# Optimization experiments

Measured on AMD Instinct MI355X. Metric: run time of the kernel, lower is better.

The kernel has to match this reference:

```python
import jax, jax.numpy as jnp
import numpy as np

N = 8192
D_IN, D_GAT, D_GCN = 128, 64, 64


def setup_inputs() -> dict:
    key = jax.random.key(0)
    ks = jax.random.split(key, 7)
    feat = jax.random.normal(ks[0], (N, D_IN), dtype=jnp.float32)
    r = jax.random.uniform(ks[1], (N, N), dtype=jnp.float32)
    sup = jnp.where(r < 0.01, r * 100.0, 0.0)
    xav = lambda k, shape: jax.random.normal(k, shape, dtype=jnp.float32) * jnp.sqrt(2.0 / (shape[0] + shape[1]))
    W_map = xav(ks[2], (D_IN, D_GAT))
    b_map = jnp.zeros((1,), dtype=jnp.float32)
    U = xav(ks[3], (D_GAT, 1))
    V = xav(ks[4], (D_GAT, 1))
    W_gcn = xav(ks[5], (D_GAT, D_GCN))
    return {"feat": feat, "sup": sup, "W_map": W_map, "b_map": b_map, "U": U, "V": V, "W_gcn": W_gcn}


def reference(feat, sup, W_map, b_map, U, V, W_gcn):
    n = sup.shape[0]
    sup2 = sup + jnp.eye(n, dtype=sup.dtype)  # add self-loops
    # GAT layer
    h = feat @ W_map                            # [N, D_GAT]
    s = h @ U                                   # [N, 1] score from source node i
    t = h @ V                                   # [N, 1] score from target node j
    # torch loop builds att[j, i] = tanh(s_i + t_j + b)
    att = jnp.tanh(s.T + t + b_map)             # [N, N]
    att = jnp.where(sup2 > 0, att, jnp.float32(-100.0))
    att = jax.nn.softmax(att, axis=1)
    gat_feat = jnp.tanh(att @ h)                # [N, D_GAT]
    # GCN layer (dropout is identity at inference)
    agg = sup2 @ gat_feat                       # [N, D_GAT]
    out = jax.nn.relu(agg @ W_gcn)              # [N, D_GCN]
    norm = jnp.linalg.norm(out, axis=1, keepdims=True)
    out = out / jnp.maximum(norm, jnp.float32(1e-12))  # F.normalize(p=2, dim=1)
    return out
```

## Files before the change

### kernel.cpp

```cpp
#include <hip/hip_runtime.h>
#include <hip/hip_bf16.h>


#define N_NODES 8192
#define D_IN    128
#define D_GAT   64
#define SLOTS   256
#define K1_BLOCKS (N_NODES / 4)

__global__ __launch_bounds__(256) void k12_map_compact(
    const float* __restrict__ feat, const float* __restrict__ W_map,
    const float* __restrict__ U, const float* __restrict__ V,
    const float* __restrict__ sup,
    float* __restrict__ h, float* __restrict__ s, float* __restrict__ t,
    int* __restrict__ cnt, int* __restrict__ col, float* __restrict__ val)
{
    if (blockIdx.x < K1_BLOCKS) {
        const int r = threadIdx.x >> 6;
        const int d = threadIdx.x & 63;
        const int row = blockIdx.x * 4 + r;
        __shared__ float f[4 * D_IN];
        if (threadIdx.x < 128)
            ((float4*)f)[threadIdx.x] =
                ((const float4*)(feat + (size_t)blockIdx.x * 4 * D_IN))[threadIdx.x];
        __syncthreads();
        const float* fr = f + r * D_IN;
        float acc = 0.f;
#pragma unroll 8
        for (int k = 0; k < D_IN; ++k)
            acc += fr[k] * W_map[k * D_GAT + d];
        h[row * D_GAT + d] = acc;
        float sv = acc * U[d];
        float tv = acc * V[d];
#pragma unroll
        for (int off = 32; off > 0; off >>= 1) {
            sv += __shfl_xor(sv, off);
            tv += __shfl_xor(tv, off);
        }
        if (d == 0) { s[row] = sv; t[row] = tv; }
    } else {
        const int j = blockIdx.x - K1_BLOCKS;
        const int lane = threadIdx.x & 63;
        __shared__ int c;
        if (threadIdx.x == 0) c = 0;
        __syncthreads();
        const float4* row = (const float4*)(sup + (size_t)j * N_NODES);
        int*   colj = col + j * SLOTS;
        float* valj = val + j * SLOTS;
        for (int q = threadIdx.x; q < N_NODES / 4; q += 256) {
            float4 v = row[q];
            const int i0 = q * 4;
            float vs[4] = {v.x, v.y, v.z, v.w};
#pragma unroll
            for (int u = 0; u < 4; ++u) {
                const int i = i0 + u;
                const float vv = vs[u] + ((i == j) ? 1.0f : 0.0f);
                const bool keep = vv > 0.f;
                const unsigned long long mask = __ballot(keep);
                if (mask) {
                    int base = 0;
                    if (lane == 0) base = atomicAdd(&c, __popcll(mask));
                    base = __shfl(base, 0);
                    if (keep) {
                        const int pos = base +
                            __popcll(mask & ((1ull << lane) - 1ull));
                        if (pos < SLOTS) { colj[pos] = i; valj[pos] = vv; }
                    }
                }
            }
        }
        __syncthreads();
        if (threadIdx.x == 0) cnt[j] = (c < SLOTS) ? c : SLOTS;
    }
}

__global__ __launch_bounds__(256) void k3_gat(
    const float* __restrict__ h, const float* __restrict__ s,
    const float* __restrict__ t, const float* __restrict__ b,
    const int* __restrict__ cnt, const int* __restrict__ col,
    float* __restrict__ gat)
{
    const int wid  = threadIdx.x >> 6;
    const int lane = threadIdx.x & 63;
    const int j = blockIdx.x * 4 + wid;
    const int m = cnt[j];
    const int* colj = col + j * SLOTS;
    __shared__ int   cl_s[4][SLOTS];
    __shared__ float w_s[4][SLOTS];
    int*   cl = cl_s[wid];
    float* w  = w_s[wid];
    const float tj = t[j] + b[0];

    float lmax = -1e30f;
    for (int p = lane; p < m; p += 64) {
        const int ci = colj[p];
        cl[p] = ci;
        const float e = tanhf(s[ci] + tj);
        w[p] = e;
        lmax = fmaxf(lmax, e);
    }
#pragma unroll
    for (int off = 32; off > 0; off >>= 1)
        lmax = fmaxf(lmax, __shfl_xor(lmax, off));

    float lsum = 0.f;
    for (int p = lane; p < m; p += 64) {
        const float e = __expf(w[p] - lmax);
        w[p] = e;
        lsum += e;
    }
#pragma unroll
    for (int off = 32; off > 0; off >>= 1) lsum += __shfl_xor(lsum, off);
    __syncthreads();

    const int c16 = (lane & 15) * 4;
    const int pp  = lane >> 4;
    float4 a0 = make_float4(0,0,0,0), a1 = a0, a2 = a0, a3 = a0;
    for (int base = 0; base < m; base += 16) {
        const int p0 = base + pp, p1 = p0 + 4, p2 = p0 + 8, p3 = p0 + 12;
        if (p0 < m) { const float wp = w[p0];
            const float4 v = *(const float4*)(h + cl[p0] * D_GAT + c16);
            a0.x += wp*v.x; a0.y += wp*v.y; a0.z += wp*v.z; a0.w += wp*v.w; }
        if (p1 < m) { const float wp = w[p1];
            const float4 v = *(const float4*)(h + cl[p1] * D_GAT + c16);
            a1.x += wp*v.x; a1.y += wp*v.y; a1.z += wp*v.z; a1.w += wp*v.w; }
        if (p2 < m) { const float wp = w[p2];
            const float4 v = *(const float4*)(h + cl[p2] * D_GAT + c16);
            a2.x += wp*v.x; a2.y += wp*v.y; a2.z += wp*v.z; a2.w += wp*v.w; }
        if (p3 < m) { const float wp = w[p3];
            const float4 v = *(const float4*)(h + cl[p3] * D_GAT + c16);
            a3.x += wp*v.x; a3.y += wp*v.y; a3.z += wp*v.z; a3.w += wp*v.w; }
    }
    float4 acc;
    acc.x = (a0.x + a1.x) + (a2.x + a3.x);
    acc.y = (a0.y + a1.y) + (a2.y + a3.y);
    acc.z = (a0.z + a1.z) + (a2.z + a3.z);
    acc.w = (a0.w + a1.w) + (a2.w + a3.w);
#pragma unroll
    for (int off = 16; off <= 32; off <<= 1) {
        acc.x += __shfl_xor(acc.x, off); acc.y += __shfl_xor(acc.y, off);
        acc.z += __shfl_xor(acc.z, off); acc.w += __shfl_xor(acc.w, off);
    }
    if (pp == 0) {
        const float inv = 1.0f / lsum;
        float4 o;
        o.x = tanhf(acc.x * inv); o.y = tanhf(acc.y * inv);
        o.z = tanhf(acc.z * inv); o.w = tanhf(acc.w * inv);
        *(float4*)(gat + j * D_GAT + c16) = o;
    }
}

__global__ __launch_bounds__(256) void k4_gcn(
    const float* __restrict__ gat, const float* __restrict__ W_gcn,
    const int* __restrict__ cnt, const int* __restrict__ col,
    const float* __restrict__ val, float* __restrict__ out)
{
    const int wid  = threadIdx.x >> 6;
    const int lane = threadIdx.x & 63;
    const int j = blockIdx.x * 4 + wid;
    const int m = cnt[j];
    const int*   colj = col + j * SLOTS;
    const float* valj = val + j * SLOTS;
    __shared__ int   cl_s[4][SLOTS];
    __shared__ float wv_s[4][SLOTS];
    __shared__ float a_s[4][D_GAT];
    int*   cl = cl_s[wid];
    float* wv = wv_s[wid];
    float* a  = a_s[wid];
    for (int p = lane; p < m; p += 64) { cl[p] = colj[p]; wv[p] = valj[p]; }
    __syncthreads();

    const int c16 = (lane & 15) * 4;
    const int pp  = lane >> 4;
    float4 a0 = make_float4(0,0,0,0), a1 = a0, a2 = a0, a3 = a0;
    for (int base = 0; base < m; base += 16) {
        const int p0 = base + pp, p1 = p0 + 4, p2 = p0 + 8, p3 = p0 + 12;
        if (p0 < m) { const float wp = wv[p0];
            const float4 v = *(const float4*)(gat + cl[p0] * D_GAT + c16);
            a0.x += wp*v.x; a0.y += wp*v.y; a0.z += wp*v.z; a0.w += wp*v.w; }
        if (p1 < m) { const float wp = wv[p1];
            const float4 v = *(const float4*)(gat + cl[p1] * D_GAT + c16);
            a1.x += wp*v.x; a1.y += wp*v.y; a1.z += wp*v.z; a1.w += wp*v.w; }
        if (p2 < m) { const float wp = wv[p2];
            const float4 v = *(const float4*)(gat + cl[p2] * D_GAT + c16);
            a2.x += wp*v.x; a2.y += wp*v.y; a2.z += wp*v.z; a2.w += wp*v.w; }
        if (p3 < m) { const float wp = wv[p3];
            const float4 v = *(const float4*)(gat + cl[p3] * D_GAT + c16);
            a3.x += wp*v.x; a3.y += wp*v.y; a3.z += wp*v.z; a3.w += wp*v.w; }
    }
    float4 acc;
    acc.x = (a0.x + a1.x) + (a2.x + a3.x);
    acc.y = (a0.y + a1.y) + (a2.y + a3.y);
    acc.z = (a0.z + a1.z) + (a2.z + a3.z);
    acc.w = (a0.w + a1.w) + (a2.w + a3.w);
#pragma unroll
    for (int off = 16; off <= 32; off <<= 1) {
        acc.x += __shfl_xor(acc.x, off); acc.y += __shfl_xor(acc.y, off);
        acc.z += __shfl_xor(acc.z, off); acc.w += __shfl_xor(acc.w, off);
    }
    if (pp == 0) *(float4*)(a + c16) = acc;
    __syncthreads();

    float o = 0.f;
#pragma unroll 8
    for (int d = 0; d < D_GAT; ++d)
        o += a[d] * W_gcn[d * D_GAT + lane];
    o = fmaxf(o, 0.f);

    float ss = o * o;
#pragma unroll
    for (int off = 32; off > 0; off >>= 1) ss += __shfl_xor(ss, off);
    const float nrm = sqrtf(ss);
    out[j * D_GAT + lane] = o / fmaxf(nrm, 1e-12f);
}

extern "C" void kernel_launch(void* const* d_in, const int* in_sizes, int n_in,
                              void* d_out, int out_size, void* d_ws, size_t ws_size,
                              hipStream_t stream) {
    const float* feat  = (const float*)d_in[0];
    const float* sup   = (const float*)d_in[1];
    const float* W_map = (const float*)d_in[2];
    const float* b_map = (const float*)d_in[3];
    const float* U     = (const float*)d_in[4];
    const float* V     = (const float*)d_in[5];
    const float* W_gcn = (const float*)d_in[6];
    float* out = (float*)d_out;

    char* ws = (char*)d_ws;
    float* h   = (float*)(ws);
    float* gat = (float*)(ws + (2u << 20));
    float* s   = (float*)(ws + (4u << 20));
    float* t   = (float*)(ws + (4u << 20) + 32768);
    int*   cnt = (int*)  (ws + (4u << 20) + 65536);
    int*   col = (int*)  (ws + (4u << 20) + 98304);
    float* val = (float*)(ws + (12u << 20) + 98304);

    k12_map_compact<<<K1_BLOCKS + N_NODES, 256, 0, stream>>>(
        feat, W_map, U, V, sup, h, s, t, cnt, col, val);
    k3_gat<<<N_NODES / 4, 256, 0, stream>>>(h, s, t, b_map, cnt, col, gat);
    k4_gcn<<<N_NODES / 4, 256, 0, stream>>>(gat, W_gcn, cnt, col, val, out);
}
```

Before: 408.8 us.

## Compact adjacency per-wave segments without shared atomics, issue all row loads upfront

The sparse-compaction stage now gives each of the four waves its own 64-slot segment of a row with a per-wave count, so the shared-memory atomic, the broadcast shuffle and the block barriers go away. Each wave issues its eight float4 loads of the dense row before processing them, which raises memory-level parallelism on the 256 MB adjacency scan. The consumer kernels merge the four segments into shared memory using the per-wave counts. The risk is that a wave's segment overflows and silently drops edges if more than 64 nonzeros fall in a 2048-column chunk, where before the limit was 256 per row.

```diff
diff --git a/kernel.cpp b/kernel.cpp
--- a/kernel.cpp
+++ b/kernel.cpp
@@ -6,6 +6,7 @@
 #define D_IN    128
 #define D_GAT   64
 #define SLOTS   256
+#define SEG     64
 #define K1_BLOCKS (N_NODES / 4)
 
 __global__ __launch_bounds__(256) void k12_map_compact(
@@ -13,7 +14,7 @@
     const float* __restrict__ U, const float* __restrict__ V,
     const float* __restrict__ sup,
     float* __restrict__ h, float* __restrict__ s, float* __restrict__ t,
-    int* __restrict__ cnt, int* __restrict__ col, float* __restrict__ val)
+    int* __restrict__ cnt4, int* __restrict__ col, float* __restrict__ val)
 {
     if (blockIdx.x < K1_BLOCKS) {
         const int r = threadIdx.x >> 6;
@@ -39,51 +40,51 @@
         }
         if (d == 0) { s[row] = sv; t[row] = tv; }
     } else {
-        const int j = blockIdx.x - K1_BLOCKS;
+        const int j    = blockIdx.x - K1_BLOCKS;
+        const int w    = threadIdx.x >> 6;
         const int lane = threadIdx.x & 63;
-        __shared__ int c;
-        if (threadIdx.x == 0) c = 0;
-        __syncthreads();
         const float4* row = (const float4*)(sup + (size_t)j * N_NODES);
-        int*   colj = col + j * SLOTS;
-        float* valj = val + j * SLOTS;
-        for (int q = threadIdx.x; q < N_NODES / 4; q += 256) {
-            float4 v = row[q];
-            const int i0 = q * 4;
-            float vs[4] = {v.x, v.y, v.z, v.w};
+        int*   colw = col + j * SLOTS + w * SEG;
+        float* valw = val + j * SLOTS + w * SEG;
+
+        float4 v[8];
+#pragma unroll
+        for (int it = 0; it < 8; ++it)
+            v[it] = row[w * 512 + it * 64 + lane];
+
+        int cw = 0;
+        const unsigned long long ltmask = (lane == 63) ? ~0ull >> 1
+                                        : (1ull << lane) - 1ull;
+#pragma unroll
+        for (int it = 0; it < 8; ++it) {
+            const int i0 = (w * 512 + it * 64 + lane) * 4;
+            const float vs[4] = {v[it].x, v[it].y, v[it].z, v[it].w};
 #pragma unroll
             for (int u = 0; u < 4; ++u) {
                 const int i = i0 + u;
                 const float vv = vs[u] + ((i == j) ? 1.0f : 0.0f);
                 const bool keep = vv > 0.f;
                 const unsigned long long mask = __ballot(keep);
-                if (mask) {
-                    int base = 0;
-                    if (lane == 0) base = atomicAdd(&c, __popcll(mask));
-                    base = __shfl(base, 0);
-                    if (keep) {
-                        const int pos = base +
-                            __popcll(mask & ((1ull << lane) - 1ull));
-                        if (pos < SLOTS) { colj[pos] = i; valj[pos] = vv; }
-                    }
+                if (keep) {
+                    const int pos = cw + __popcll(mask & ltmask);
+                    if (pos < SEG) { colw[pos] = i; valw[pos] = vv; }
                 }
+                cw += __popcll(mask);
             }
         }
-        __syncthreads();
-        if (threadIdx.x == 0) cnt[j] = (c < SLOTS) ? c : SLOTS;
+        if (lane == 0) cnt4[j * 4 + w] = (cw < SEG) ? cw : SEG;
     }
 }
 
 __global__ __launch_bounds__(256) void k3_gat(
     const float* __restrict__ h, const float* __restrict__ s,
     const float* __restrict__ t, const float* __restrict__ b,
-    const int* __restrict__ cnt, const int* __restrict__ col,
+    const int* __restrict__ cnt4, const int* __restrict__ col,
     float* __restrict__ gat)
 {
     const int wid  = threadIdx.x >> 6;
     const int lane = threadIdx.x & 63;
     const int j = blockIdx.x * 4 + wid;
-    const int m = cnt[j];
     const int* colj = col + j * SLOTS;
     __shared__ int   cl_s[4][SLOTS];
     __shared__ float w_s[4][SLOTS];
@@ -91,11 +92,17 @@
     float* w  = w_s[wid];
     const float tj = t[j] + b[0];
 
+    int m = 0;
+#pragma unroll
+    for (int k = 0; k < 4; ++k) {
+        const int ck = cnt4[j * 4 + k];
+        if (lane < ck) cl[m + lane] = colj[k * SEG + lane];
+        m += ck;
+    }
+
     float lmax = -1e30f;
     for (int p = lane; p < m; p += 64) {
-        const int ci = colj[p];
-        cl[p] = ci;
-        const float e = tanhf(s[ci] + tj);
+        const float e = tanhf(s[cl[p]] + tj);
         w[p] = e;
         lmax = fmaxf(lmax, e);
     }
@@ -119,17 +126,17 @@
     for (int base = 0; base < m; base += 16) {
         const int p0 = base + pp, p1 = p0 + 4, p2 = p0 + 8, p3 = p0 + 12;
         if (p0 < m) { const float wp = w[p0];
-            const float4 v = *(const float4*)(h + cl[p0] * D_GAT + c16);
-            a0.x += wp*v.x; a0.y += wp*v.y; a0.z += wp*v.z; a0.w += wp*v.w; }
+            const float4 hv = *(const float4*)(h + cl[p0] * D_GAT + c16);
+            a0.x += wp*hv.x; a0.y += wp*hv.y; a0.z += wp*hv.z; a0.w += wp*hv.w; }
         if (p1 < m) { const float wp = w[p1];
-            const float4 v = *(const float4*)(h + cl[p1] * D_GAT + c16);
-            a1.x += wp*v.x; a1.y += wp*v.y; a1.z += wp*v.z; a1.w += wp*v.w; }
+            const float4 hv = *(const float4*)(h + cl[p1] * D_GAT + c16);
+            a1.x += wp*hv.x; a1.y += wp*hv.y; a1.z += wp*hv.z; a1.w += wp*hv.w; }
         if (p2 < m) { const float wp = w[p2];
-            const float4 v = *(const float4*)(h + cl[p2] * D_GAT + c16);
-            a2.x += wp*v.x; a2.y += wp*v.y; a2.z += wp*v.z; a2.w += wp*v.w; }
+            const float4 hv = *(const float4*)(h + cl[p2] * D_GAT + c16);
+            a2.x += wp*hv.x; a2.y += wp*hv.y; a2.z += wp*hv.z; a2.w += wp*hv.w; }
         if (p3 < m) { const float wp = w[p3];
-            const float4 v = *(const float4*)(h + cl[p3] * D_GAT + c16);
-            a3.x += wp*v.x; a3.y += wp*v.y; a3.z += wp*v.z; a3.w += wp*v.w; }
+            const float4 hv = *(const float4*)(h + cl[p3] * D_GAT + c16);
+            a3.x += wp*hv.x; a3.y += wp*hv.y; a3.z += wp*hv.z; a3.w += wp*hv.w; }
     }
     float4 acc;
     acc.x = (a0.x + a1.x) + (a2.x + a3.x);
@@ -152,13 +159,12 @@
 
 __global__ __launch_bounds__(256) void k4_gcn(
     const float* __restrict__ gat, const float* __restrict__ W_gcn,
-    const int* __restrict__ cnt, const int* __restrict__ col,
+    const int* __restrict__ cnt4, const int* __restrict__ col,
     const float* __restrict__ val, float* __restrict__ out)
 {
     const int wid  = threadIdx.x >> 6;
     const int lane = threadIdx.x & 63;
     const int j = blockIdx.x * 4 + wid;
-    const int m = cnt[j];
     const int*   colj = col + j * SLOTS;
     const float* valj = val + j * SLOTS;
     __shared__ int   cl_s[4][SLOTS];
@@ -167,7 +173,17 @@
     int*   cl = cl_s[wid];
     float* wv = wv_s[wid];
     float* a  = a_s[wid];
-    for (int p = lane; p < m; p += 64) { cl[p] = colj[p]; wv[p] = valj[p]; }
+
+    int m = 0;
+#pragma unroll
+    for (int k = 0; k < 4; ++k) {
+        const int ck = cnt4[j * 4 + k];
+        if (lane < ck) {
+            cl[m + lane] = colj[k * SEG + lane];
+            wv[m + lane] = valj[k * SEG + lane];
+        }
+        m += ck;
+    }
     __syncthreads();
 
     const int c16 = (lane & 15) * 4;
@@ -176,17 +192,17 @@
     for (int base = 0; base < m; base += 16) {
         const int p0 = base + pp, p1 = p0 + 4, p2 = p0 + 8, p3 = p0 + 12;
         if (p0 < m) { const float wp = wv[p0];
-            const float4 v = *(const float4*)(gat + cl[p0] * D_GAT + c16);
-            a0.x += wp*v.x; a0.y += wp*v.y; a0.z += wp*v.z; a0.w += wp*v.w; }
+            const float4 gv = *(const float4*)(gat + cl[p0] * D_GAT + c16);
+            a0.x += wp*gv.x; a0.y += wp*gv.y; a0.z += wp*gv.z; a0.w += wp*gv.w; }
         if (p1 < m) { const float wp = wv[p1];
-            const float4 v = *(const float4*)(gat + cl[p1] * D_GAT + c16);
-            a1.x += wp*v.x; a1.y += wp*v.y; a1.z += wp*v.z; a1.w += wp*v.w; }
+            const float4 gv = *(const float4*)(gat + cl[p1] * D_GAT + c16);
+            a1.x += wp*gv.x; a1.y += wp*gv.y; a1.z += wp*gv.z; a1.w += wp*gv.w; }
         if (p2 < m) { const float wp = wv[p2];
-            const float4 v = *(const float4*)(gat + cl[p2] * D_GAT + c16);
-            a2.x += wp*v.x; a2.y += wp*v.y; a2.z += wp*v.z; a2.w += wp*v.w; }
+            const float4 gv = *(const float4*)(gat + cl[p2] * D_GAT + c16);
+            a2.x += wp*gv.x; a2.y += wp*gv.y; a2.z += wp*gv.z; a2.w += wp*gv.w; }
         if (p3 < m) { const float wp = wv[p3];
-            const float4 v = *(const float4*)(gat + cl[p3] * D_GAT + c16);
-            a3.x += wp*v.x; a3.y += wp*v.y; a3.z += wp*v.z; a3.w += wp*v.w; }
+            const float4 gv = *(const float4*)(gat + cl[p3] * D_GAT + c16);
+            a3.x += wp*gv.x; a3.y += wp*gv.y; a3.z += wp*gv.z; a3.w += wp*gv.w; }
     }
     float4 acc;
     acc.x = (a0.x + a1.x) + (a2.x + a3.x);
@@ -227,16 +243,16 @@
     float* out = (float*)d_out;
 
     char* ws = (char*)d_ws;
-    float* h   = (float*)(ws);
-    float* gat = (float*)(ws + (2u << 20));
-    float* s   = (float*)(ws + (4u << 20));
-    float* t   = (float*)(ws + (4u << 20) + 32768);
-    int*   cnt = (int*)  (ws + (4u << 20) + 65536);
-    int*   col = (int*)  (ws + (4u << 20) + 98304);
-    float* val = (float*)(ws + (12u << 20) + 98304);
+    float* h    = (float*)(ws);
+    float* gat  = (float*)(ws + (2u << 20));
+    float* s    = (float*)(ws + (4u << 20));
+    float* t    = (float*)(ws + (4u << 20) + 32768);
+    int*   cnt4 = (int*)  (ws + (4u << 20) + 65536);
+    int*   col  = (int*)  (ws + (5u << 20));
+    float* val  = (float*)(ws + (13u << 20));
 
     k12_map_compact<<<K1_BLOCKS + N_NODES, 256, 0, stream>>>(
-        feat, W_map, U, V, sup, h, s, t, cnt, col, val);
-    k3_gat<<<N_NODES / 4, 256, 0, stream>>>(h, s, t, b_map, cnt, col, gat);
-    k4_gcn<<<N_NODES / 4, 256, 0, stream>>>(gat, W_gcn, cnt, col, val, out);
-}
+        feat, W_map, U, V, sup, h, s, t, cnt4, col, val);
+    k3_gat<<<N_NODES / 4, 256, 0, stream>>>(h, s, t, b_map, cnt4, col, gat);
+    k4_gcn<<<N_NODES / 4, 256, 0, stream>>>(gat, W_gcn, cnt4, col, val, out);
+}
```

Measured after the change: 414.3 us. No clear change (+1.3%).
